# Kernel optimization log

Hardware: AMD Instinct MI355X
Metric: run time of the kernel (lower is better)

## Reference

```python
import jax, jax.numpy as jnp
import numpy as np

B, T, DM, H, DQ, FF, L, OUT = 4, 512, 768, 8, 32, 3072, 6, 80
D_REL = 100   # relative_positional_distance
NEG = 1e8
LN_EPS = 1e-5


def _layer_norm(x, w, b):
    mu = jnp.mean(x, axis=-1, keepdims=True)
    var = jnp.mean((x - mu) ** 2, axis=-1, keepdims=True)
    return (x - mu) * jax.lax.rsqrt(var + LN_EPS) * w + b


def _attention(x, wq, wk, wv, wo, rel):
    # x: (B,T,DM); wq/wk/wv: (H,DM,DQ); wo: (H,DQ,DM); rel: (H, 2*D_REL-1, DQ)
    Tq = x.shape[1]
    q = jnp.einsum('btf,hfa->bhta', x, wq) / (DQ ** 0.5)   # q pre-scaled (as in source)
    k = jnp.einsum('btf,hfa->bhta', x, wk)
    v = jnp.einsum('btf,hfa->bhta', x, wv)
    logits = jnp.einsum('bhqa,bhka->bhqk', q, k)

    # relative positional logits over the 199 learned offsets
    rel_log = jnp.einsum('bhqd,hmd->bhqm', q, rel)          # (B,H,T,2*D_REL-1)
    pad = Tq - D_REL
    if pad > 0:
        # zero-pad to 2T-1 rel positions, then mask out-of-range offsets with -1e8
        rel_log = jnp.pad(rel_log, ((0, 0), (0, 0), (0, 0), (pad, pad)))
        m = jnp.arange(2 * Tq - 1)
        oob = (m < pad) | (m >= 2 * Tq - 1 - pad)
        rel_log = rel_log - NEG * oob.astype(rel_log.dtype)
    else:
        start = D_REL - Tq
        rel_log = rel_log[..., start:start + 2 * Tq - 1]
    # relative -> absolute indexing: pos[..., i, j] = rel_log[..., i, (j - i) + T - 1]
    idx = jnp.arange(Tq)[None, :] - jnp.arange(Tq)[:, None] + (Tq - 1)   # (T,T)
    pos = jnp.take_along_axis(rel_log, idx[None, None], axis=-1)         # (B,H,T,T)

    probs = jax.nn.softmax(logits + pos, axis=-1)
    o = jnp.einsum('bhqk,bhka->bhqa', probs, v)
    return jnp.einsum('bhta,had->btd', o, wo)


def _forward(x, wq, wk, wv, wo, rel, lin1_w, lin1_b, lin2_w, lin2_b,
             ln1_w, ln1_b, ln2_w, ln2_b, w_out, b_out):
    def step(h, p):
        (q, k, v, o, r, l1w, l1b, l2w, l2b, n1w, n1b, n2w, n2b) = p
        a = _attention(h, q, k, v, o, r)
        h = _layer_norm(h + a, n1w, n1b)                  # post-norm, residual
        ff = jnp.maximum(h @ l1w.T + l1b, 0.0) @ l2w.T + l2b
        h = _layer_norm(h + ff, n2w, n2b)
        return h, None
    h, _ = jax.lax.scan(step, x, (wq, wk, wv, wo, rel, lin1_w, lin1_b,
                                  lin2_w, lin2_b, ln1_w, ln1_b, ln2_w, ln2_b))
    return h @ w_out.T + b_out                            # (B,T,OUT)


def setup_inputs() -> dict:
    key = jax.random.key(0)
    ks = jax.random.split(key, 16)
    n = lambda k, shape, scale: (jax.random.normal(k, shape, dtype=jnp.float32) * scale)
    s_qkv = (2.0 / (DM + DQ)) ** 0.5      # xavier_normal_ scale
    s_o = (2.0 / (DQ + DM)) ** 0.5
    return {
        'x':      n(ks[0], (B, T, DM), 1.0),
        'wq':     n(ks[1], (L, H, DM, DQ), s_qkv),
        'wk':     n(ks[2], (L, H, DM, DQ), s_qkv),
        'wv':     n(ks[3], (L, H, DM, DQ), s_qkv),
        'wo':     n(ks[4], (L, H, DQ, DM), s_o),
        'rel':    n(ks[5], (L, H, 2 * D_REL - 1, DQ), DQ ** -0.5),
        'lin1_w': n(ks[6], (L, FF, DM), DM ** -0.5),
        'lin1_b': jnp.zeros((L, FF), jnp.float32),
        'lin2_w': n(ks[7], (L, DM, FF), FF ** -0.5),
        'lin2_b': jnp.zeros((L, DM), jnp.float32),
        'ln1_w':  jnp.ones((L, DM), jnp.float32),
        'ln1_b':  jnp.zeros((L, DM), jnp.float32),
        'ln2_w':  jnp.ones((L, DM), jnp.float32),
        'ln2_b':  jnp.zeros((L, DM), jnp.float32),
        'w_out':  n(ks[8], (OUT, DM), DM ** -0.5),
        'b_out':  jnp.zeros((OUT,), jnp.float32),
    }


def reference(x, wq, wk, wv, wo, rel, lin1_w, lin1_b, lin2_w, lin2_b,
              ln1_w, ln1_b, ln2_w, ln2_b, w_out, b_out):
    return _forward(x, wq, wk, wv, wo, rel, lin1_w, lin1_b, lin2_w, lin2_b,
                    ln1_w, ln1_b, ln2_w, ln2_b, w_out, b_out)
```

## Files before the change

### kernel.cpp

```cpp
#include <hip/hip_runtime.h>

typedef _Float16 f16;
typedef f16 f16x8 __attribute__((ext_vector_type(8)));
typedef f16 f16x4 __attribute__((ext_vector_type(4)));
typedef float f32x4 __attribute__((ext_vector_type(4)));

#define B_ 4
#define T_ 512
#define DM_ 768
#define H_ 8
#define DQ_ 32
#define FF_ 3072
#define L_ 6
#define OUT_ 80
#define M_ (B_*T_)

__device__ __forceinline__ void gload16(const f16* g, f16* l) {
    __builtin_amdgcn_global_load_lds(
        (const __attribute__((address_space(1))) unsigned int*)g,
        (__attribute__((address_space(3))) unsigned int*)l, 16, 0, 0);
}

template<int N> __device__ __forceinline__ void wait_vm() {
    if constexpr (N == 0)      asm volatile("s_waitcnt vmcnt(0)" ::: "memory");
    else if constexpr (N == 3) asm volatile("s_waitcnt vmcnt(3)" ::: "memory");
    else if constexpr (N == 4) asm volatile("s_waitcnt vmcnt(4)" ::: "memory");
    else if constexpr (N == 6) asm volatile("s_waitcnt vmcnt(6)" ::: "memory");
    else                       asm volatile("s_waitcnt vmcnt(0)" ::: "memory");
}


#define PKU_X  98304L
#define PKU_L1 (PKU_X + 884736L)
#define PKU_L2 (PKU_L1 + 884736L)
#define PKB_VEC 7296
#define PKB_LIN 1632
#define PKB_QKV 1728
#define PKB_WO  1152
#define PKB_TOTAL (PKB_VEC + PKB_LIN + PKB_QKV + PKB_WO)

__global__ void pack_all_kernel(
    const float* __restrict__ x, const float* __restrict__ wq, const float* __restrict__ wk,
    const float* __restrict__ wv, const float* __restrict__ wo, const float* __restrict__ rel,
    const float* __restrict__ lin1w, const float* __restrict__ lin2w, const float* __restrict__ wout,
    f16* __restrict__ xH, f16* __restrict__ BTqkv, f16* __restrict__ BTwo,
    f16* __restrict__ lin1H, f16* __restrict__ lin2H, f16* __restrict__ woutH, f16* __restrict__ relH)
{
    __shared__ float tile[64 * 33];
    const int bid = blockIdx.x, tid = threadIdx.x;
    if (bid < PKB_VEC) {
        const long u = (long)bid * 256 + tid;
        const float* src; f16* dst; long off;
        if (u < PKU_X)       { src = x;     dst = xH;    off = u; }
        else if (u < PKU_L1) { src = lin1w; dst = lin1H; off = u - PKU_X; }
        else                 { src = lin2w; dst = lin2H; off = u - PKU_L1; }
        const float4 v0 = ((const float4*)src)[off * 4];
        const float4 v1 = ((const float4*)src)[off * 4 + 1];
        const float4 v2 = ((const float4*)src)[off * 4 + 2];
        const float4 v3 = ((const float4*)src)[off * 4 + 3];
        f16x8 o0, o1;
        o0[0] = (f16)v0.x; o0[1] = (f16)v0.y; o0[2] = (f16)v0.z; o0[3] = (f16)v0.w;
        o0[4] = (f16)v1.x; o0[5] = (f16)v1.y; o0[6] = (f16)v1.z; o0[7] = (f16)v1.w;
        o1[0] = (f16)v2.x; o1[1] = (f16)v2.y; o1[2] = (f16)v2.z; o1[3] = (f16)v2.w;
        o1[4] = (f16)v3.x; o1[5] = (f16)v3.y; o1[6] = (f16)v3.z; o1[7] = (f16)v3.w;
        ((f16x8*)dst)[off * 2]     = o0;
        ((f16x8*)dst)[off * 2 + 1] = o1;
    } else if (bid < PKB_VEC + PKB_LIN) {
        const long u = (long)(bid - PKB_VEC) * 256 + tid;
        if (u < 98304) {
            const int k = (int)(u % 768), n = (int)(u / 768);
            woutH[u] = (n < OUT_) ? (f16)wout[n * 768 + k] : (f16)0;
        } else {
            const long v2 = u - 98304;
            const int a = (int)(v2 & 31);
            const long t = v2 >> 5;
            const int d = (int)(t % 208);
            const int lh = (int)(t / 208);
            relH[v2] = (d < 199) ? (f16)rel[((long)lh * 199 + d) * 32 + a] : (f16)0;
        }
    } else if (bid < PKB_VEC + PKB_LIN + PKB_QKV) {
        const int g = bid - (PKB_VEC + PKB_LIN);
        const int kb = g % 12;
        const int grp = g / 12;
        const int h = grp & 7, sec = (grp >> 3) % 3, l = grp / 24;
        const float* w = (sec == 0) ? wq : (sec == 1 ? wk : wv);
        const float* src = w + (((long)l * 8 + h) * 768 + kb * 64) * 32;
        const float scale = (sec == 0) ? 0.17677669529663687f : 1.f;
#pragma unroll
        for (int p = 0; p < 2; ++p) {
            const int kk = p * 32 + (tid >> 3), a = (tid & 7) * 4;
            const float4 v = *(const float4*)(src + (long)kk * 32 + a);
            tile[kk * 33 + a]     = v.x * scale;
            tile[kk * 33 + a + 1] = v.y * scale;
            tile[kk * 33 + a + 2] = v.z * scale;
            tile[kk * 33 + a + 3] = v.w * scale;
        }
        __syncthreads();
        f16* dst = BTqkv + ((long)l * 768 + sec * 256 + h * 32) * 768 + kb * 64;
        {
            const int a = tid >> 3, k8 = (tid & 7) * 8;
            f16x8 o;
#pragma unroll
            for (int e = 0; e < 8; ++e) o[e] = (f16)tile[(k8 + e) * 33 + a];
            *(f16x8*)(dst + (long)a * 768 + k8) = o;
        }
    } else {
        const int g = bid - (PKB_VEC + PKB_LIN + PKB_QKV);
        const int nb = g % 24;
        const int tmp = g / 24;
        const int kb2 = tmp % 8, l = tmp / 8;
        const float* src = wo + ((long)l * 256 + kb2 * 32) * 768 + nb * 32;
        {
            const int r = tid >> 3, c = (tid & 7) * 4;
            const float4 v = *(const float4*)(src + (long)r * 768 + c);
            tile[r * 33 + c]     = v.x;
            tile[r * 33 + c + 1] = v.y;
            tile[r * 33 + c + 2] = v.z;
            tile[r * 33 + c + 3] = v.w;
        }
        __syncthreads();
        if (tid < 128) {
            const int n = tid >> 2, k8 = (tid & 3) * 8;
            f16x8 o;
#pragma unroll
            for (int e = 0; e < 8; ++e) o[e] = (f16)tile[(k8 + e) * 33 + n];
            f16* dst = BTwo + ((long)l * 768 + nb * 32 + n) * 256 + kb2 * 32 + k8;
            *(f16x8*)dst = o;
        }
    }
}

__device__ __forceinline__ void xcd_tile(int BM, int BN, int& m0, int& n0) {
    const int gx = gridDim.x;
    const int id = blockIdx.y * gx + blockIdx.x;
    const int cpx = (gx * gridDim.y) >> 3;
    const int t = (id & 7) * cpx + (id >> 3);
    m0 = (t / gx) * BM;
    n0 = (t % gx) * BN;
}


template<int BM, int BN>
__global__ __launch_bounds__(256) void gemm7_kernel(
    const f16* __restrict__ A, const f16* __restrict__ Bt,
    const float* __restrict__ bias, const float* __restrict__ res,
    float* __restrict__ outF, f16* __restrict__ outH, f16* __restrict__ vTout,
    int M, int N, int K, int mode, int ldOut, int nMax)
{
    constexpr int IA = BM / 32;
    constexpr int JF = BN / 32;
    constexpr int LA = BM / 32;
    constexpr int LB = BN / 32;
    constexpr int L  = LA + LB;
    __shared__ __align__(16) f16 As[2][BM * 64];
    __shared__ __align__(16) f16 Bs[2][BN * 64];
    const int tid = threadIdx.x;
    const int wave = tid >> 6, lane = tid & 63;
    int m0, n0; xcd_tile(BM, BN, m0, n0);
    const int z = blockIdx.z;
    const int Kl = K / (int)gridDim.z;
    const int kb = z * Kl;
    const int nt = Kl / 64;
    const int wr = wave >> 1, wc = wave & 1;
    const int l15 = lane & 15, l4 = lane >> 4;
    const int lrow = lane >> 3;
    const int lcol = ((lane & 7) ^ (lane >> 3)) * 8;

    const f16* Abase = A  + (long)(m0 + lrow) * K + kb + lcol;
    const f16* Bbase = Bt + (long)(n0 + lrow) * K + kb + lcol;

    f32x4 acc[IA][JF];
#pragma unroll
    for (int i = 0; i < IA; ++i)
#pragma unroll
        for (int j = 0; j < JF; ++j) acc[i][j] = (f32x4){0.f, 0.f, 0.f, 0.f};

    auto stage = [&](int buf, int k0) {
#pragma unroll
        for (int i = 0; i < LA; ++i) {
            const int c = wave + 4 * i;
            gload16(Abase + (long)c * 8 * K + k0, &As[buf][c * 512]);
        }
#pragma unroll
        for (int i = 0; i < LB; ++i) {
            const int c = wave + 4 * i;
            gload16(Bbase + (long)c * 8 * K + k0, &Bs[buf][c * 512]);
        }
    };

    stage(0, 0);
    int cur = 0;
    for (int t = 0; t < nt; ++t) {
        if (t + 1 < nt) { stage(cur ^ 1, (t + 1) * 64); wait_vm<L>(); }
        else            { wait_vm<0>(); }
        __builtin_amdgcn_s_barrier();
#pragma unroll
        for (int s = 0; s < 2; ++s) {
            f16x8 af[IA], bf[JF];
#pragma unroll
            for (int i = 0; i < IA; ++i) {
                const int row = wr * (BM / 2) + i * 16 + l15;
                af[i] = *(const f16x8*)&As[cur][row * 64 + (((s * 4 + l4) ^ (l15 & 7)) * 8)];
            }
#pragma unroll
            for (int j = 0; j < JF; ++j) {
                const int row = wc * (BN / 2) + j * 16 + l15;
                bf[j] = *(const f16x8*)&Bs[cur][row * 64 + (((s * 4 + l4) ^ (l15 & 7)) * 8)];
            }
#pragma unroll
            for (int i = 0; i < IA; ++i)
#pragma unroll
                for (int j = 0; j < JF; ++j)
                    acc[i][j] = __builtin_amdgcn_mfma_f32_16x16x32_f16(af[i], bf[j], acc[i][j], 0, 0, 0);
        }
        __builtin_amdgcn_s_barrier();
        cur ^= 1;
    }

#pragma unroll
    for (int i = 0; i < IA; ++i) {
#pragma unroll
        for (int j = 0; j < JF; ++j) {
            const int col = n0 + wc * (BN / 2) + j * 16 + l15;
            if (mode & 32) {
#pragma unroll
                for (int r = 0; r < 4; ++r) {
                    const int row = m0 + wr * (BM / 2) + i * 16 + l4 * 4 + r;
                    float v = acc[i][j][r];
                    if (col < 512) {
                        outH[(long)row * 512 + col] = (f16)v;
                    } else {
                        const int bb = row >> 9, t = row & 511;
                        vTout[((long)(bb * 256 + (col - 512))) * 512 + t] = (f16)v;
                    }
                }
            } else if (mode & 64) {
                f16* po = outH + (long)z * M * ldOut;
#pragma unroll
                for (int r = 0; r < 4; ++r) {
                    const int row = m0 + wr * (BM / 2) + i * 16 + l4 * 4 + r;
                    po[(long)row * ldOut + col] = (f16)acc[i][j][r];
                }
            } else if (col < nMax) {
                const float bvv = (mode & 1) ? bias[col] : 0.f;
#pragma unroll
                for (int r = 0; r < 4; ++r) {
                    const int row = m0 + wr * (BM / 2) + i * 16 + l4 * 4 + r;
                    float v = acc[i][j][r] + bvv;
                    if (mode & 2) v += res[(long)row * N + col];
                    if (mode & 4) v = fmaxf(v, 0.f);
                    if (mode & 8)  outF[(long)row * ldOut + col] = v;
                    if (mode & 16) outH[(long)row * ldOut + col] = (f16)v;
                }
            }
        }
    }
}


__global__ __launch_bounds__(256) void attn_kernel(
    const f16* __restrict__ qkvH, const f16* __restrict__ vT,
    const f16* __restrict__ relH, int l, f16* __restrict__ o)
{
    __shared__ __align__(16) f16 Ks[272 * 40];
    __shared__ __align__(16) f16 Vt[32 * 296];
    __shared__ __align__(16) f16 Scr[64 * 296];
    const int tid = threadIdx.x;
    const int qb = blockIdx.x, h = blockIdx.y, b = blockIdx.z;
    const int q0 = qb * 64;
    int lo = q0 - 99; lo = (lo > 0) ? (lo & ~7) : 0;
    const int hi = min(512, q0 + 163);
    const int nk = hi - lo;

    for (int idx = tid; idx < 272 * 4; idx += 256) {
        const int r = idx >> 2, c = idx & 3;
        f16x8 v = {};
        if (r < nk)
            v = *(const f16x8*)(qkvH + ((long)(b * 512 + lo + r)) * 512 + 256 + h * 32 + c * 8);
        *(f16x8*)&Ks[r * 40 + c * 8] = v;
    }
    for (int idx = tid; idx < 32 * 36; idx += 256) {
        const int a = idx / 36, k8 = idx % 36;
        f16x8 v = {};
        const int kbase = k8 * 8;
        if (kbase < nk) {
            const f16* src = vT + ((long)(b * 256 + h * 32 + a)) * 512 + lo + kbase;
            if (kbase + 8 <= nk) {
                v = *(const f16x8*)src;
            } else {
#pragma unroll
                for (int e = 0; e < 8; ++e) if (kbase + e < nk) v[e] = src[e];
            }
        }
        *(f16x8*)&Vt[a * 296 + kbase] = v;
    }

    const int wave = tid >> 6, lane = tid & 63;
    const int l15 = lane & 15, l4 = lane >> 4;
    const int qloc = wave * 16;

    const f16x8 qf = *(const f16x8*)(qkvH + ((long)(b * 512 + q0 + qloc + l15)) * 512 + h * 32 + l4 * 8);

    const f16* relh = relH + ((long)(l * 8 + h)) * 208 * 32;
    {
        f32x4 racc[13];
#pragma unroll
        for (int fd = 0; fd < 13; ++fd) {
            const f16x8 bf = *(const f16x8*)(relh + (fd * 16 + l15) * 32 + l4 * 8);
            racc[fd] = __builtin_amdgcn_mfma_f32_16x16x32_f16(qf, bf, (f32x4){0.f,0.f,0.f,0.f}, 0, 0, 0);
        }
#pragma unroll
        for (int fd = 0; fd < 13; ++fd)
#pragma unroll
            for (int r = 0; r < 4; ++r)
                Scr[(qloc + l4 * 4 + r) * 296 + fd * 16 + l15] = (f16)racc[fd][r];
    }
    __syncthreads();

    f32x4 sacc[17];
#pragma unroll
    for (int fk = 0; fk < 17; ++fk) {
        const f16x8 bf = *(const f16x8*)&Ks[(fk * 16 + l15) * 40 + l4 * 8];
        sacc[fk] = __builtin_amdgcn_mfma_f32_16x16x32_f16(qf, bf, (f32x4){0.f,0.f,0.f,0.f}, 0, 0, 0);
    }

    float mx[4] = {-1e30f, -1e30f, -1e30f, -1e30f};
#pragma unroll
    for (int fk = 0; fk < 17; ++fk) {
        const int kk = fk * 16 + l15;
        const int k = lo + kk;
#pragma unroll
        for (int r = 0; r < 4; ++r) {
            const int q = q0 + qloc + l4 * 4 + r;
            const int d = k - q + 99;
            float v = -1e30f;
            if (kk < nk && d >= 0 && d < 199)
                v = sacc[fk][r] + (float)Scr[(qloc + l4 * 4 + r) * 296 + d];
            sacc[fk][r] = v;
            mx[r] = fmaxf(mx[r], v);
        }
    }
#pragma unroll
    for (int r = 0; r < 4; ++r) {
        mx[r] = fmaxf(mx[r], __shfl_xor(mx[r], 1));
        mx[r] = fmaxf(mx[r], __shfl_xor(mx[r], 2));
        mx[r] = fmaxf(mx[r], __shfl_xor(mx[r], 4));
        mx[r] = fmaxf(mx[r], __shfl_xor(mx[r], 8));
    }
    float sum[4] = {0.f, 0.f, 0.f, 0.f};
#pragma unroll
    for (int fk = 0; fk < 17; ++fk) {
        const int kk = fk * 16 + l15;
#pragma unroll
        for (int r = 0; r < 4; ++r) {
            const float p = __expf(sacc[fk][r] - mx[r]);
            sum[r] += p;
            Scr[(qloc + l4 * 4 + r) * 296 + kk] = (f16)p;
        }
    }
#pragma unroll
    for (int r = 0; r < 4; ++r)
        Scr[(qloc + l4 * 4 + r) * 296 + 272 + l15] = (f16)0;
#pragma unroll
    for (int r = 0; r < 4; ++r) {
        sum[r] += __shfl_xor(sum[r], 1);
        sum[r] += __shfl_xor(sum[r], 2);
        sum[r] += __shfl_xor(sum[r], 4);
        sum[r] += __shfl_xor(sum[r], 8);
    }

    f32x4 oacc[2] = {{0.f,0.f,0.f,0.f}, {0.f,0.f,0.f,0.f}};
#pragma unroll
    for (int ks = 0; ks < 9; ++ks) {
        const f16x8 pa = *(const f16x8*)&Scr[(qloc + l15) * 296 + ks * 32 + l4 * 8];
#pragma unroll
        for (int j = 0; j < 2; ++j) {
            const f16x8 vb = *(const f16x8*)&Vt[(j * 16 + l15) * 296 + ks * 32 + l4 * 8];
            oacc[j] = __builtin_amdgcn_mfma_f32_16x16x32_f16(pa, vb, oacc[j], 0, 0, 0);
        }
    }

    f16* ob = o + ((long)(b * 512 + q0 + qloc + l4 * 4)) * 256 + h * 32;
#pragma unroll
    for (int r = 0; r < 4; ++r) {
        const float inv = 1.f / sum[r];
#pragma unroll
        for (int j = 0; j < 2; ++j)
            ob[(long)r * 256 + j * 16 + l15] = (f16)(oacc[j][r] * inv);
    }
}


__global__ __launch_bounds__(256) void ln_kernel(
    const float* __restrict__ src, const float* __restrict__ w, const float* __restrict__ bb,
    float* __restrict__ outF, f16* __restrict__ outH)
{
    __shared__ float red1[4], red2[4];
    const int row = blockIdx.x, tid = threadIdx.x;
    const float* x = src + (long)row * 768;
    float v0 = x[tid], v1 = x[tid + 256], v2 = x[tid + 512];
    float s = v0 + v1 + v2;
#pragma unroll
    for (int off = 32; off > 0; off >>= 1) s += __shfl_xor(s, off);
    if ((tid & 63) == 0) red1[tid >> 6] = s;
    __syncthreads();
    const float mu = (red1[0] + red1[1] + red1[2] + red1[3]) * (1.f / 768.f);
    const float d0 = v0 - mu, d1 = v1 - mu, d2 = v2 - mu;
    float ss = d0 * d0 + d1 * d1 + d2 * d2;
#pragma unroll
    for (int off = 32; off > 0; off >>= 1) ss += __shfl_xor(ss, off);
    if ((tid & 63) == 0) red2[tid >> 6] = ss;
    __syncthreads();
    const float var = (red2[0] + red2[1] + red2[2] + red2[3]) * (1.f / 768.f);
    const float inv = rsqrtf(var + 1e-5f);
    float y0 = d0 * inv * w[tid]       + bb[tid];
    float y1 = d1 * inv * w[tid + 256] + bb[tid + 256];
    float y2 = d2 * inv * w[tid + 512] + bb[tid + 512];
    long base = (long)row * 768;
    outF[base + tid] = y0; outF[base + tid + 256] = y1; outF[base + tid + 512] = y2;
    outH[base + tid] = (f16)y0; outH[base + tid + 256] = (f16)y1; outH[base + tid + 512] = (f16)y2;
}


__global__ __launch_bounds__(256) void ln_sum4_kernel(
    const f16* __restrict__ p,
    const float* __restrict__ bias, const float* __restrict__ res,
    const float* __restrict__ w, const float* __restrict__ bb,
    float* __restrict__ outF, f16* __restrict__ outH)
{
    __shared__ float red1[4], red2[4];
    const int row = blockIdx.x, tid = threadIdx.x;
    const long rb = (long)row * 768;
    float v[3];
#pragma unroll
    for (int i = 0; i < 3; ++i) {
        const int c = tid + i * 256;
        float s = bias[c] + res[rb + c];
#pragma unroll
        for (int zz = 0; zz < 4; ++zz) s += (float)p[((long)zz * M_ + row) * 768 + c];
        v[i] = s;
    }
    float s = v[0] + v[1] + v[2];
#pragma unroll
    for (int off = 32; off > 0; off >>= 1) s += __shfl_xor(s, off);
    if ((tid & 63) == 0) red1[tid >> 6] = s;
    __syncthreads();
    const float mu = (red1[0] + red1[1] + red1[2] + red1[3]) * (1.f / 768.f);
    const float d0 = v[0] - mu, d1 = v[1] - mu, d2 = v[2] - mu;
    float ss = d0 * d0 + d1 * d1 + d2 * d2;
#pragma unroll
    for (int off = 32; off > 0; off >>= 1) ss += __shfl_xor(ss, off);
    if ((tid & 63) == 0) red2[tid >> 6] = ss;
    __syncthreads();
    const float var = (red2[0] + red2[1] + red2[2] + red2[3]) * (1.f / 768.f);
    const float inv = rsqrtf(var + 1e-5f);
    float y0 = d0 * inv * w[tid]       + bb[tid];
    float y1 = d1 * inv * w[tid + 256] + bb[tid + 256];
    float y2 = d2 * inv * w[tid + 512] + bb[tid + 512];
    outF[rb + tid] = y0; outF[rb + tid + 256] = y1; outF[rb + tid + 512] = y2;
    outH[rb + tid] = (f16)y0; outH[rb + tid + 256] = (f16)y1; outH[rb + tid + 512] = (f16)y2;
}


extern "C" void kernel_launch(void* const* d_in, const int* in_sizes, int n_in,
                              void* d_out, int out_size, void* d_ws, size_t ws_size,
                              hipStream_t stream) {
    const float* x     = (const float*)d_in[0];
    const float* wq    = (const float*)d_in[1];
    const float* wk    = (const float*)d_in[2];
    const float* wv    = (const float*)d_in[3];
    const float* wo    = (const float*)d_in[4];
    const float* rel   = (const float*)d_in[5];
    const float* lin1w = (const float*)d_in[6];
    const float* lin1b = (const float*)d_in[7];
    const float* lin2w = (const float*)d_in[8];
    const float* lin2b = (const float*)d_in[9];
    const float* ln1w  = (const float*)d_in[10];
    const float* ln1b  = (const float*)d_in[11];
    const float* ln2w  = (const float*)d_in[12];
    const float* ln2b  = (const float*)d_in[13];
    const float* wout  = (const float*)d_in[14];
    const float* bout  = (const float*)d_in[15];

    char* base = (char*)d_ws;
    size_t off = 0;
    auto alloc = [&](size_t bytes) {
        void* p = base + off;
        off = (off + bytes + 255) & ~(size_t)255;
        return p;
    };
    f16*   xH    = (f16*)  alloc((size_t)M_ * 768 * 2);
    f16*   BTqkv = (f16*)  alloc((size_t)L_ * 768 * 768 * 2);
    f16*   BTwo  = (f16*)  alloc((size_t)L_ * 768 * 256 * 2);
    f16*   lin1H = (f16*)  alloc((size_t)L_ * 3072 * 768 * 2);
    f16*   lin2H = (f16*)  alloc((size_t)L_ * 768 * 3072 * 2);
    f16*   woutH = (f16*)  alloc((size_t)128 * 768 * 2);
    f16*   relH  = (f16*)  alloc((size_t)L_ * 8 * 208 * 32 * 2);
    f16*   qkvH  = (f16*)  alloc((size_t)M_ * 512 * 2);
    f16*   vTbuf = (f16*)  alloc((size_t)B_ * 256 * 512 * 2);
    float* scrF  = (float*)alloc((size_t)M_ * 768 * 4);
    f16*   partH = (f16*)  alloc((size_t)4 * M_ * 768 * 2);
    f16*   oH    = (f16*)  alloc((size_t)M_ * 256 * 2);
    float* ln1F  = (float*)alloc((size_t)M_ * 768 * 4);
    f16*   ln1H  = (f16*)  alloc((size_t)M_ * 768 * 2);
    f16*   ffH   = (f16*)  alloc((size_t)M_ * 3072 * 2);
    float* hF    = (float*)alloc((size_t)M_ * 768 * 4);
    f16*   hH    = (f16*)  alloc((size_t)M_ * 768 * 2);
    (void)ws_size; (void)in_sizes; (void)n_in; (void)out_size;

    pack_all_kernel<<<PKB_TOTAL, 256, 0, stream>>>(
        x, wq, wk, wv, wo, rel, lin1w, lin2w, wout,
        xH, BTqkv, BTwo, lin1H, lin2H, woutH, relH);

    for (int l = 0; l < L_; ++l) {
        const f16*   aIn   = (l == 0) ? xH : hH;
        const float* resIn = (l == 0) ? x  : hF;
        gemm7_kernel<64, 64><<<dim3(12, 32, 1), 256, 0, stream>>>(
            aIn, BTqkv + (size_t)l * 768 * 768, nullptr, nullptr, nullptr, qkvH, vTbuf,
            M_, 768, 768, 32, 512, 768);
        attn_kernel<<<dim3(8, 8, 4), 256, 0, stream>>>(qkvH, vTbuf, relH, l, oH);
        gemm7_kernel<64, 64><<<dim3(12, 32, 1), 256, 0, stream>>>(
            oH, BTwo + (size_t)l * 768 * 256, nullptr, resIn, scrF, nullptr, nullptr,
            M_, 768, 256, 2 | 8, 768, 768);
        ln_kernel<<<M_, 256, 0, stream>>>(scrF, ln1w + l * 768, ln1b + l * 768, ln1F, ln1H);
        gemm7_kernel<128, 64><<<dim3(48, 16, 1), 256, 0, stream>>>(
            ln1H, lin1H + (size_t)l * 3072 * 768, lin1b + l * 3072, nullptr, nullptr, ffH, nullptr,
            M_, 3072, 768, 1 | 4 | 16, 3072, 3072);
        gemm7_kernel<128, 64><<<dim3(12, 16, 4), 256, 0, stream>>>(
            ffH, lin2H + (size_t)l * 768 * 3072, nullptr, nullptr, nullptr, partH, nullptr,
            M_, 768, 3072, 64, 768, 768);
        ln_sum4_kernel<<<M_, 256, 0, stream>>>(partH, lin2b + l * 768, ln1F,
                                               ln2w + l * 768, ln2b + l * 768, hF, hH);
    }
    gemm7_kernel<32, 64><<<dim3(2, 64, 1), 256, 0, stream>>>(
        hH, woutH, bout, nullptr, (float*)d_out, nullptr, nullptr,
        M_, 80, 768, 1 | 8, 80, 80);
}
```

Before: 523.9 us.

## Pack two QKV heads per transpose block and shrink QKV/Wo GEMM row tiles

The weight-pack kernel now transposes two heads per block through a wider 64x65 shared tile, halving the number of QKV pack blocks and writing 64-row slabs. The QKV and output-projection GEMMs switch from 64x64 to 32x64 tiles with twice as many blocks, to fill more compute units on these small-K GEMMs. Smaller tiles lower per-block reuse of the B operand and raise redundant weight loads.

```diff
diff --git a/kernel.cpp b/kernel.cpp
--- a/kernel.cpp
+++ b/kernel.cpp
@@ -35,7 +35,7 @@
 #define PKU_L2 (PKU_L1 + 884736L)
 #define PKB_VEC 7296
 #define PKB_LIN 1632
-#define PKB_QKV 1728
+#define PKB_QKV 864
 #define PKB_WO  1152
 #define PKB_TOTAL (PKB_VEC + PKB_LIN + PKB_QKV + PKB_WO)
 
@@ -46,7 +46,7 @@
     f16* __restrict__ xH, f16* __restrict__ BTqkv, f16* __restrict__ BTwo,
     f16* __restrict__ lin1H, f16* __restrict__ lin2H, f16* __restrict__ woutH, f16* __restrict__ relH)
 {
-    __shared__ float tile[64 * 33];
+    __shared__ float tile[64 * 65];
     const int bid = blockIdx.x, tid = threadIdx.x;
     if (bid < PKB_VEC) {
         const long u = (long)bid * 256 + tid;
@@ -82,27 +82,29 @@
         const int g = bid - (PKB_VEC + PKB_LIN);
         const int kb = g % 12;
         const int grp = g / 12;
-        const int h = grp & 7, sec = (grp >> 3) % 3, l = grp / 24;
+        const int hp = grp & 3, sec = (grp >> 2) % 3, l = grp / 12;
         const float* w = (sec == 0) ? wq : (sec == 1 ? wk : wv);
-        const float* src = w + (((long)l * 8 + h) * 768 + kb * 64) * 32;
         const float scale = (sec == 0) ? 0.17677669529663687f : 1.f;
 #pragma unroll
+        for (int hh = 0; hh < 2; ++hh) {
+            const float* src = w + (((long)l * 8 + hp * 2 + hh) * 768 + kb * 64) * 32;
+#pragma unroll
+            for (int p = 0; p < 2; ++p) {
+                const int kk = p * 32 + (tid >> 3), a = (tid & 7) * 4;
+                const float4 v = *(const float4*)(src + (long)kk * 32 + a);
+                float* t = &tile[kk * 65 + hh * 32 + a];
+                t[0] = v.x * scale; t[1] = v.y * scale; t[2] = v.z * scale; t[3] = v.w * scale;
+            }
+        }
+        __syncthreads();
+        f16* dst = BTqkv + ((long)l * 768 + sec * 256 + hp * 64) * 768 + kb * 64;
+#pragma unroll
         for (int p = 0; p < 2; ++p) {
-            const int kk = p * 32 + (tid >> 3), a = (tid & 7) * 4;
-            const float4 v = *(const float4*)(src + (long)kk * 32 + a);
-            tile[kk * 33 + a]     = v.x * scale;
-            tile[kk * 33 + a + 1] = v.y * scale;
-            tile[kk * 33 + a + 2] = v.z * scale;
-            tile[kk * 33 + a + 3] = v.w * scale;
-        }
-        __syncthreads();
-        f16* dst = BTqkv + ((long)l * 768 + sec * 256 + h * 32) * 768 + kb * 64;
-        {
-            const int a = tid >> 3, k8 = (tid & 7) * 8;
+            const int nn = p * 32 + (tid >> 3), k8 = (tid & 7) * 8;
             f16x8 o;
 #pragma unroll
-            for (int e = 0; e < 8; ++e) o[e] = (f16)tile[(k8 + e) * 33 + a];
-            *(f16x8*)(dst + (long)a * 768 + k8) = o;
+            for (int e = 0; e < 8; ++e) o[e] = (f16)tile[(k8 + e) * 65 + nn];
+            *(f16x8*)(dst + (long)nn * 768 + k8) = o;
         }
     } else {
         const int g = bid - (PKB_VEC + PKB_LIN + PKB_QKV);
@@ -113,17 +115,15 @@
         {
             const int r = tid >> 3, c = (tid & 7) * 4;
             const float4 v = *(const float4*)(src + (long)r * 768 + c);
-            tile[r * 33 + c]     = v.x;
-            tile[r * 33 + c + 1] = v.y;
-            tile[r * 33 + c + 2] = v.z;
-            tile[r * 33 + c + 3] = v.w;
+            float* t = &tile[r * 65 + c];
+            t[0] = v.x; t[1] = v.y; t[2] = v.z; t[3] = v.w;
         }
         __syncthreads();
         if (tid < 128) {
             const int n = tid >> 2, k8 = (tid & 3) * 8;
             f16x8 o;
 #pragma unroll
-            for (int e = 0; e < 8; ++e) o[e] = (f16)tile[(k8 + e) * 33 + n];
+            for (int e = 0; e < 8; ++e) o[e] = (f16)tile[(k8 + e) * 65 + n];
             f16* dst = BTwo + ((long)l * 768 + nb * 32 + n) * 256 + kb2 * 32 + k8;
             *(f16x8*)dst = o;
         }
@@ -515,11 +515,11 @@
     for (int l = 0; l < L_; ++l) {
         const f16*   aIn   = (l == 0) ? xH : hH;
         const float* resIn = (l == 0) ? x  : hF;
-        gemm7_kernel<64, 64><<<dim3(12, 32, 1), 256, 0, stream>>>(
+        gemm7_kernel<32, 64><<<dim3(12, 64, 1), 256, 0, stream>>>(
             aIn, BTqkv + (size_t)l * 768 * 768, nullptr, nullptr, nullptr, qkvH, vTbuf,
             M_, 768, 768, 32, 512, 768);
         attn_kernel<<<dim3(8, 8, 4), 256, 0, stream>>>(qkvH, vTbuf, relH, l, oH);
-        gemm7_kernel<64, 64><<<dim3(12, 32, 1), 256, 0, stream>>>(
+        gemm7_kernel<32, 64><<<dim3(12, 64, 1), 256, 0, stream>>>(
             oH, BTwo + (size_t)l * 768 * 256, nullptr, resIn, scrF, nullptr, nullptr,
             M_, 768, 256, 2 | 8, 768, 768);
         ln_kernel<<<M_, 256, 0, stream>>>(scrF, ln1w + l * 768, ln1b + l * 768, ln1F, ln1H);
```

New measurement: 501.7 us (median of 3 runs). -4.2%, faster.
